# Kernel tuning notes

Measured on AMD Instinct MI355X. Metric: run time of the kernel, lower is better.

The kernel has to match this reference:

```python
import jax, jax.numpy as jnp
import numpy as np

DIM = 384
NH = 12
DH = 32
WH = WW = 7
WS = WH * WW
SCALE = DH ** -0.5


def _relative_position_index(wh, ww):
    # replicates double_step_seq + flip + flatten from the torch module
    seq1 = np.arange(wh) * (2 * ww - 1)
    seq2 = np.arange(ww)
    coords = (seq1[:, None] + seq2[None, :]).reshape(1, -1)  # (1, ws)
    idx = coords + coords.T                                   # (ws, ws)
    idx = idx[:, ::-1]                                        # flip along dim 1
    return jnp.asarray(idx.reshape(-1), dtype=jnp.int32)      # (ws*ws,)

REL_IDX = _relative_position_index(WH, WW)


def setup_inputs() -> dict:
    key = jax.random.key(0)
    k1, k2, k3, k4, k5, k6 = jax.random.split(key, 6)
    x = jax.random.normal(k1, (2048, WS, DIM), dtype=jnp.float32)
    # 0 / -inf style shifted-window mask (use -1e9 for numerical safety)
    u = jax.random.uniform(k2, (64, WS, WS))
    mask = jnp.where(u < 0.1, -1e9, 0.0).astype(jnp.float32)
    inner = NH * DH
    w_qkv = jax.random.normal(k3, (DIM, 3 * inner), dtype=jnp.float32) * 0.02
    bias_table = jax.random.normal(k4, ((2 * WH - 1) * (2 * WW - 1), NH), dtype=jnp.float32) * 0.02
    w_out = jax.random.normal(k5, (inner, DIM), dtype=jnp.float32) * 0.02
    b_out = jax.random.normal(k6, (DIM,), dtype=jnp.float32) * 0.02
    return {"x": x, "mask": mask, "w_qkv": w_qkv, "bias_table": bias_table,
            "w_out": w_out, "b_out": b_out}


def reference(x, mask, w_qkv, bias_table, w_out, b_out):
    b, n, _ = x.shape
    qkv = x @ w_qkv                                  # (b, n, 3*nh*dh)
    q, k, v = jnp.split(qkv, 3, axis=-1)
    def to_heads(t):
        return t.reshape(b, n, NH, DH).transpose(0, 2, 1, 3)  # (b, nh, n, dh)
    q, k, v = to_heads(q) * SCALE, to_heads(k), to_heads(v)
    sim = jnp.einsum('bhid,bhjd->bhij', q, k)        # (b, nh, n, n)
    rel_bias = bias_table[REL_IDX].reshape(WS, WS, NH).transpose(2, 0, 1)  # (nh, n, n)
    sim = sim + rel_bias[None]
    nw = mask.shape[0]
    sim = sim.reshape(b // nw, nw, NH, n, n) + mask[None, :, None]
    sim = sim.reshape(b, NH, n, n)
    attn = jax.nn.softmax(sim, axis=-1)
    out = jnp.einsum('bhij,bhjd->bhid', attn, v)     # (b, nh, n, dh)
    out = out.transpose(0, 2, 1, 3).reshape(b, n, NH * DH)
    return out @ w_out + b_out
```

## Files before the change

kernel.cpp:

```cpp
#include <hip/hip_runtime.h>
#include <hip/hip_bf16.h>
#include <cstdint>
#include <cstddef>

typedef __bf16 bf16_t;
typedef __bf16 bf16x8 __attribute__((ext_vector_type(8)));
typedef __bf16 bf16x4v __attribute__((ext_vector_type(4)));
typedef float f32x4 __attribute__((ext_vector_type(4)));

#define SCALE_Q 0.17677669529663687f


__global__ void conv_x_kernel(const float* __restrict__ x, bf16_t* __restrict__ xb, int n4) {
  int i = blockIdx.x * blockDim.x + threadIdx.x;
  int stride = gridDim.x * blockDim.x;
  const float4* xv = (const float4*)x;
  for (; i < n4; i += stride) {
    float4 v = xv[i];
    bf16x4v o;
    o[0] = (bf16_t)v.x; o[1] = (bf16_t)v.y; o[2] = (bf16_t)v.z; o[3] = (bf16_t)v.w;
    *(bf16x4v*)(xb + (size_t)i * 4) = o;
  }
}

__global__ void conv_small_kernel(const float* __restrict__ w_qkv, const float* __restrict__ w_out,
                                  const float* __restrict__ bias_table, const float* __restrict__ mask,
                                  bf16_t* __restrict__ wqkvt, bf16_t* __restrict__ woutt,
                                  float* __restrict__ rbm) {
  const int N1 = 1152 * 384;
  const int N2 = 384 * 384;
  const int N3 = 64 * 12 * 2401;
  int i = blockIdx.x * blockDim.x + threadIdx.x;
  int stride = gridDim.x * blockDim.x;
  for (; i < N1 + N2 + N3; i += stride) {
    if (i < N1) {
      int n = i / 384, k = i - n * 384;
      wqkvt[i] = (bf16_t)w_qkv[k * 1152 + n];
    } else if (i < N1 + N2) {
      int j = i - N1;
      int n = j / 384, k = j - n * 384;
      woutt[j] = (bf16_t)w_out[k * 384 + n];
    } else {
      int j = i - (N1 + N2);
      int w = j / 28812; int rem = j - w * 28812;
      int h = rem / 2401; int ij = rem - h * 2401;
      int ii = ij / 49; int jj = ij - ii * 49;
      int ci = (ii / 7) * 13 + (ii % 7);
      int j48 = 48 - jj;
      int cj = (j48 / 7) * 13 + (j48 % 7);
      rbm[j] = bias_table[(ci + cj) * 12 + h] + mask[w * 2401 + ij];
    }
  }
}


__global__ __launch_bounds__(256) void gemm_qkv_kernel(const bf16_t* __restrict__ A,
                                                       const bf16_t* __restrict__ Bt,
                                                       bf16_t* __restrict__ Q, bf16_t* __restrict__ K,
                                                       bf16_t* __restrict__ V) {
  __shared__ bf16_t As[128 * 32];
  __shared__ bf16_t Bs[128 * 32];
  int bm = blockIdx.x, bn = blockIdx.y;
  int t = threadIdx.x;
  int lane = t & 63, w = t >> 6, wr = w >> 1, wc = w & 1;
  int m0 = bm * 128, n0 = bn * 128;

  int abase[2], bbase[2];
#pragma unroll
  for (int q = 0; q < 2; ++q) {
    int idx8 = q * 256 + t;
    int r = idx8 >> 2, ko = (idx8 & 3) << 3;
    abase[q] = (m0 + r) * 384 + ko;
    bbase[q] = (n0 + r) * 384 + ko;
  }

  f32x4 acc[4][4] = {};
  int lr = lane & 15, lg = lane >> 4;
  for (int kt = 0; kt < 12; ++kt) {
    int k0 = kt * 32;
#pragma unroll
    for (int q = 0; q < 2; ++q) {
      int idx8 = q * 256 + t;
      *(uint4*)(&As[idx8 * 8]) = *(const uint4*)(&A[abase[q] + k0]);
      *(uint4*)(&Bs[idx8 * 8]) = *(const uint4*)(&Bt[bbase[q] + k0]);
    }
    __syncthreads();
    bf16x8 af[4], bfv[4];
#pragma unroll
    for (int mi = 0; mi < 4; ++mi) af[mi] = *(const bf16x8*)(&As[(wr * 64 + mi * 16 + lr) * 32 + lg * 8]);
#pragma unroll
    for (int ni = 0; ni < 4; ++ni) bfv[ni] = *(const bf16x8*)(&Bs[(wc * 64 + ni * 16 + lr) * 32 + lg * 8]);
#pragma unroll
    for (int mi = 0; mi < 4; ++mi)
#pragma unroll
      for (int ni = 0; ni < 4; ++ni)
        acc[mi][ni] = __builtin_amdgcn_mfma_f32_16x16x32_bf16(af[mi], bfv[ni], acc[mi][ni], 0, 0, 0);
    __syncthreads();
  }

#pragma unroll
  for (int mi = 0; mi < 4; ++mi)
#pragma unroll
    for (int ni = 0; ni < 4; ++ni) {
      int c = n0 + wc * 64 + ni * 16 + lr;
      int part = c / 384;
      int cc = c - part * 384;
      int h = cc >> 5, d = cc & 31;
      bf16_t* dst = (part == 0) ? Q : ((part == 1) ? K : V);
      float sc = (part == 0) ? SCALE_Q : 1.0f;
#pragma unroll
      for (int rg = 0; rg < 4; ++rg) {
        int m = m0 + wr * 64 + mi * 16 + lg * 4 + rg;
        int b = m / 49; int n = m - b * 49;
        dst[((size_t)(b * 12 + h) * 49 + n) * 32 + d] = (bf16_t)(acc[mi][ni][rg] * sc);
      }
    }
}


__global__ __launch_bounds__(64) void attn_kernel(bf16_t* Qio, const bf16_t* __restrict__ Kb,
                                                  const bf16_t* __restrict__ Vb,
                                                  const float* __restrict__ rbm) {
  __shared__ float tbl[49 * 49];
  __shared__ bf16_t Pl[64 * 72];
  __shared__ bf16_t Vt[32 * 72];
  int bh = blockIdx.x;
  int b = bh / 12, h = bh - b * 12;
  int w = b & 63;
  int t = threadIdx.x;
  int lr = t & 15, lg = t >> 4;

  const float* tsrc = rbm + (size_t)(w * 12 + h) * 2401;
  for (int i = t; i < 2401; i += 64) tbl[i] = tsrc[i];
  for (int i = t; i < 32 * 72; i += 64) Vt[i] = (bf16_t)0.0f;
  __syncthreads();

  const bf16_t* vb = Vb + (size_t)bh * 1568;
  for (int ch = t; ch < 196; ch += 64) {
    int row = ch >> 2; int d8 = (ch & 3) << 3;
    bf16x8 vv = *(const bf16x8*)(&vb[row * 32 + d8]);
#pragma unroll
    for (int j = 0; j < 8; ++j) Vt[(d8 + j) * 72 + row] = vv[j];
  }

  const bf16_t* qb = Qio + (size_t)bh * 1568;
  const bf16_t* kb = Kb + (size_t)bh * 1568;
  bf16x8 aq[4], ak[4];
#pragma unroll
  for (int ti = 0; ti < 4; ++ti) { int r = ti * 16 + lr; if (r > 48) r = 48; aq[ti] = *(const bf16x8*)(&qb[r * 32 + lg * 8]); }
#pragma unroll
  for (int tj = 0; tj < 4; ++tj) { int r = tj * 16 + lr; if (r > 48) r = 48; ak[tj] = *(const bf16x8*)(&kb[r * 32 + lg * 8]); }

  f32x4 s[4][4];
#pragma unroll
  for (int ti = 0; ti < 4; ++ti)
#pragma unroll
    for (int tj = 0; tj < 4; ++tj) {
      f32x4 z = {};
      s[ti][tj] = __builtin_amdgcn_mfma_f32_16x16x32_bf16(aq[ti], ak[tj], z, 0, 0, 0);
    }

#pragma unroll
  for (int ti = 0; ti < 4; ++ti)
#pragma unroll
    for (int tj = 0; tj < 4; ++tj)
#pragma unroll
      for (int rg = 0; rg < 4; ++rg) {
        int i = ti * 16 + lg * 4 + rg;
        int j = tj * 16 + lr;
        int ic = i < 49 ? i : 48;
        float add = (j < 49) ? tbl[ic * 49 + j] : -1e30f;
        s[ti][tj][rg] += add;
      }

  float rs[4][4];
#pragma unroll
  for (int ti = 0; ti < 4; ++ti)
#pragma unroll
    for (int rg = 0; rg < 4; ++rg) {
      float mx = fmaxf(fmaxf(s[ti][0][rg], s[ti][1][rg]), fmaxf(s[ti][2][rg], s[ti][3][rg]));
#pragma unroll
      for (int off = 1; off < 16; off <<= 1) mx = fmaxf(mx, __shfl_xor(mx, off));
      float sm = 0.f;
#pragma unroll
      for (int tj = 0; tj < 4; ++tj) {
        float p = __expf(s[ti][tj][rg] - mx);
        s[ti][tj][rg] = p;
        sm += p;
      }
#pragma unroll
      for (int off = 1; off < 16; off <<= 1) sm += __shfl_xor(sm, off);
      rs[ti][rg] = 1.0f / sm;
    }

#pragma unroll
  for (int ti = 0; ti < 4; ++ti)
#pragma unroll
    for (int tj = 0; tj < 4; ++tj)
#pragma unroll
      for (int rg = 0; rg < 4; ++rg) {
        int row = ti * 16 + lg * 4 + rg, col = tj * 16 + lr;
        Pl[row * 72 + col] = (bf16_t)s[ti][tj][rg];
      }
  __syncthreads();

  f32x4 o[4][2] = {};
#pragma unroll
  for (int ks = 0; ks < 2; ++ks) {
    bf16x8 bv[2];
#pragma unroll
    for (int tn = 0; tn < 2; ++tn) bv[tn] = *(const bf16x8*)(&Vt[(tn * 16 + lr) * 72 + ks * 32 + lg * 8]);
#pragma unroll
    for (int ti = 0; ti < 4; ++ti) {
      bf16x8 ap = *(const bf16x8*)(&Pl[(ti * 16 + lr) * 72 + ks * 32 + lg * 8]);
#pragma unroll
      for (int tn = 0; tn < 2; ++tn)
        o[ti][tn] = __builtin_amdgcn_mfma_f32_16x16x32_bf16(ap, bv[tn], o[ti][tn], 0, 0, 0);
    }
  }

  bf16_t* ob = Qio + (size_t)bh * 1568;
#pragma unroll
  for (int ti = 0; ti < 4; ++ti)
#pragma unroll
    for (int tn = 0; tn < 2; ++tn)
#pragma unroll
      for (int rg = 0; rg < 4; ++rg) {
        int row = ti * 16 + lg * 4 + rg;
        if (row < 49) {
          int d = tn * 16 + lr;
          ob[row * 32 + d] = (bf16_t)(o[ti][tn][rg] * rs[ti][rg]);
        }
      }
}


__global__ __launch_bounds__(256) void gemm_out_kernel(const bf16_t* __restrict__ O,
                                                       const bf16_t* __restrict__ Bt,
                                                       const float* __restrict__ bias,
                                                       float* __restrict__ C) {
  __shared__ bf16_t As[128 * 32];
  __shared__ bf16_t Bs[128 * 32];
  int bm = blockIdx.x, bn = blockIdx.y;
  int t = threadIdx.x;
  int lane = t & 63, w = t >> 6, wr = w >> 1, wc = w & 1;
  int m0 = bm * 128, n0 = bn * 128;

  int abase[2], bbase[2];
#pragma unroll
  for (int q = 0; q < 2; ++q) {
    int idx8 = q * 256 + t;
    int r = idx8 >> 2, ko = (idx8 & 3) << 3;
    int m = m0 + r;
    int b = m / 49, n = m - b * 49;
    abase[q] = b * 18816 + n * 32 + ko;
    bbase[q] = (n0 + r) * 384 + ko;
  }

  f32x4 acc[4][4] = {};
  int lr = lane & 15, lg = lane >> 4;
  for (int kt = 0; kt < 12; ++kt) {
#pragma unroll
    for (int q = 0; q < 2; ++q) {
      int idx8 = q * 256 + t;
      *(uint4*)(&As[idx8 * 8]) = *(const uint4*)(&O[abase[q] + kt * 1568]);
      *(uint4*)(&Bs[idx8 * 8]) = *(const uint4*)(&Bt[bbase[q] + kt * 32]);
    }
    __syncthreads();
    bf16x8 af[4], bfv[4];
#pragma unroll
    for (int mi = 0; mi < 4; ++mi) af[mi] = *(const bf16x8*)(&As[(wr * 64 + mi * 16 + lr) * 32 + lg * 8]);
#pragma unroll
    for (int ni = 0; ni < 4; ++ni) bfv[ni] = *(const bf16x8*)(&Bs[(wc * 64 + ni * 16 + lr) * 32 + lg * 8]);
#pragma unroll
    for (int mi = 0; mi < 4; ++mi)
#pragma unroll
      for (int ni = 0; ni < 4; ++ni)
        acc[mi][ni] = __builtin_amdgcn_mfma_f32_16x16x32_bf16(af[mi], bfv[ni], acc[mi][ni], 0, 0, 0);
    __syncthreads();
  }

#pragma unroll
  for (int mi = 0; mi < 4; ++mi)
#pragma unroll
    for (int ni = 0; ni < 4; ++ni) {
      int c = n0 + wc * 64 + ni * 16 + lr;
      float bo = bias[c];
#pragma unroll
      for (int rg = 0; rg < 4; ++rg) {
        int m = m0 + wr * 64 + mi * 16 + lg * 4 + rg;
        C[(size_t)m * 384 + c] = acc[mi][ni][rg] + bo;
      }
    }
}


extern "C" void kernel_launch(void* const* d_in, const int* in_sizes, int n_in,
                              void* d_out, int out_size, void* d_ws, size_t ws_size,
                              hipStream_t stream) {
  const float* x          = (const float*)d_in[0];
  const float* mask       = (const float*)d_in[1];
  const float* w_qkv      = (const float*)d_in[2];
  const float* bias_table = (const float*)d_in[3];
  const float* w_out      = (const float*)d_in[4];
  const float* b_out      = (const float*)d_in[5];
  float* out = (float*)d_out;

  const size_t XE = 38535168ULL;
  char* ws = (char*)d_ws;
  size_t off = 0;
  auto alloc = [&](size_t bytes) { void* p = ws + off; off += (bytes + 255) & ~(size_t)255; return p; };
  bf16_t* xb    = (bf16_t*)alloc(XE * 2);
  bf16_t* wqkvt = (bf16_t*)alloc(442368ULL * 2);
  bf16_t* woutt = (bf16_t*)alloc(147456ULL * 2);
  float*  rbm   = (float*) alloc(1843968ULL * 4);
  bf16_t* Qb    = (bf16_t*)alloc(XE * 2);
  bf16_t* Kb    = (bf16_t*)alloc(XE * 2);
  bf16_t* Vb    = (bf16_t*)alloc(XE * 2);
  if (off > ws_size) return;

  conv_x_kernel<<<2048, 256, 0, stream>>>(x, xb, (int)(XE / 4));
  conv_small_kernel<<<1188, 256, 0, stream>>>(w_qkv, w_out, bias_table, mask, wqkvt, woutt, rbm);
  gemm_qkv_kernel<<<dim3(784, 9), 256, 0, stream>>>(xb, wqkvt, Qb, Kb, Vb);
  attn_kernel<<<24576, 64, 0, stream>>>(Qb, Kb, Vb, rbm);
  gemm_out_kernel<<<dim3(784, 3), 256, 0, stream>>>(Qb, woutt, b_out, out);
}
```

Baseline: 704.7 us.

## Use direct global-to-LDS loads, swizzle block order, and persist attention per window-head

Both GEMM kernels now stage tiles with global_load_lds instead of register round-trips, and remap a flattened 1D block id in an XCD-aware order for better L2 locality. The attention kernel becomes persistent per (window, head): each 128-thread block loads the bias+mask table once and two waves each loop over 16 batches, instead of reloading the 2401-entry table for every (batch, head). In exchange there are fewer blocks (768), so less parallelism to hide latency, plus a per-wave LDS dependency that relies on an explicit waitcnt rather than a barrier.

```diff
diff --git a/kernel.cpp b/kernel.cpp
--- a/kernel.cpp
+++ b/kernel.cpp
@@ -9,6 +9,12 @@
 typedef float f32x4 __attribute__((ext_vector_type(4)));
 
 #define SCALE_Q 0.17677669529663687f
+
+typedef const __attribute__((address_space(1))) unsigned int* gas1;
+typedef __attribute__((address_space(3))) unsigned int* las3;
+__device__ __forceinline__ void gload16(const bf16_t* g, bf16_t* l) {
+  __builtin_amdgcn_global_load_lds((gas1)(const void*)g, (las3)(void*)l, 16, 0, 0);
+}
 
 
 __global__ void conv_x_kernel(const float* __restrict__ x, bf16_t* __restrict__ xb, int n4) {
@@ -58,9 +64,11 @@
                                                        const bf16_t* __restrict__ Bt,
                                                        bf16_t* __restrict__ Q, bf16_t* __restrict__ K,
                                                        bf16_t* __restrict__ V) {
-  __shared__ bf16_t As[128 * 32];
-  __shared__ bf16_t Bs[128 * 32];
-  int bm = blockIdx.x, bn = blockIdx.y;
+  __shared__ __align__(16) bf16_t As[128 * 32];
+  __shared__ __align__(16) bf16_t Bs[128 * 32];
+  int bid = blockIdx.x;
+  int nb = (bid & 7) * 882 + (bid >> 3);
+  int bm = nb / 9, bn = nb - bm * 9;
   int t = threadIdx.x;
   int lane = t & 63, w = t >> 6, wr = w >> 1, wc = w & 1;
   int m0 = bm * 128, n0 = bn * 128;
@@ -78,12 +86,10 @@
   int lr = lane & 15, lg = lane >> 4;
   for (int kt = 0; kt < 12; ++kt) {
     int k0 = kt * 32;
-#pragma unroll
-    for (int q = 0; q < 2; ++q) {
-      int idx8 = q * 256 + t;
-      *(uint4*)(&As[idx8 * 8]) = *(const uint4*)(&A[abase[q] + k0]);
-      *(uint4*)(&Bs[idx8 * 8]) = *(const uint4*)(&Bt[bbase[q] + k0]);
-    }
+    gload16(&A[abase[0] + k0], &As[t * 8]);
+    gload16(&A[abase[1] + k0], &As[(256 + t) * 8]);
+    gload16(&Bt[bbase[0] + k0], &Bs[t * 8]);
+    gload16(&Bt[bbase[1] + k0], &Bs[(256 + t) * 8]);
     __syncthreads();
     bf16x8 af[4], bfv[4];
 #pragma unroll
@@ -118,120 +124,132 @@
 }
 
 
-__global__ __launch_bounds__(64) void attn_kernel(bf16_t* Qio, const bf16_t* __restrict__ Kb,
-                                                  const bf16_t* __restrict__ Vb,
-                                                  const float* __restrict__ rbm) {
-  __shared__ float tbl[49 * 49];
-  __shared__ bf16_t Pl[64 * 72];
-  __shared__ bf16_t Vt[32 * 72];
-  int bh = blockIdx.x;
-  int b = bh / 12, h = bh - b * 12;
-  int w = b & 63;
+__global__ __launch_bounds__(128) void attn_kernel(bf16_t* Qio, const bf16_t* __restrict__ Kb,
+                                                   const bf16_t* __restrict__ Vb,
+                                                   const float* __restrict__ rbm) {
+  __shared__ float tbl[2401];
+  __shared__ __align__(16) bf16_t Pl[2][64 * 72];
+  __shared__ __align__(16) bf16_t Vt[2][32 * 72];
+  int wh = blockIdx.x;
   int t = threadIdx.x;
-  int lr = t & 15, lg = t >> 4;
-
-  const float* tsrc = rbm + (size_t)(w * 12 + h) * 2401;
-  for (int i = t; i < 2401; i += 64) tbl[i] = tsrc[i];
-  for (int i = t; i < 32 * 72; i += 64) Vt[i] = (bf16_t)0.0f;
+  int wv = t >> 6, lane = t & 63;
+  int lr = lane & 15, lg = lane >> 4;
+  int w = wh / 12, h = wh - w * 12;
+
+  const float* tsrc = rbm + (size_t)wh * 2401;
+  for (int i = t; i < 2401; i += 128) tbl[i] = tsrc[i];
+  bf16_t* pl = Pl[wv];
+  bf16_t* vt = Vt[wv];
+  for (int i = lane; i < 32 * 24; i += 64) {
+    int r = i / 24, c = 48 + (i - (i / 24) * 24);
+    vt[r * 72 + c] = (bf16_t)0.0f;
+  }
   __syncthreads();
 
-  const bf16_t* vb = Vb + (size_t)bh * 1568;
-  for (int ch = t; ch < 196; ch += 64) {
-    int row = ch >> 2; int d8 = (ch & 3) << 3;
-    bf16x8 vv = *(const bf16x8*)(&vb[row * 32 + d8]);
-#pragma unroll
-    for (int j = 0; j < 8; ++j) Vt[(d8 + j) * 72 + row] = vv[j];
-  }
-
-  const bf16_t* qb = Qio + (size_t)bh * 1568;
-  const bf16_t* kb = Kb + (size_t)bh * 1568;
-  bf16x8 aq[4], ak[4];
-#pragma unroll
-  for (int ti = 0; ti < 4; ++ti) { int r = ti * 16 + lr; if (r > 48) r = 48; aq[ti] = *(const bf16x8*)(&qb[r * 32 + lg * 8]); }
-#pragma unroll
-  for (int tj = 0; tj < 4; ++tj) { int r = tj * 16 + lr; if (r > 48) r = 48; ak[tj] = *(const bf16x8*)(&kb[r * 32 + lg * 8]); }
-
-  f32x4 s[4][4];
-#pragma unroll
-  for (int ti = 0; ti < 4; ++ti)
-#pragma unroll
-    for (int tj = 0; tj < 4; ++tj) {
-      f32x4 z = {};
-      s[ti][tj] = __builtin_amdgcn_mfma_f32_16x16x32_bf16(aq[ti], ak[tj], z, 0, 0, 0);
-    }
-
-#pragma unroll
-  for (int ti = 0; ti < 4; ++ti)
-#pragma unroll
-    for (int tj = 0; tj < 4; ++tj)
+  for (int it = 0; it < 16; ++it) {
+    int b = w + 64 * (wv * 16 + it);
+    size_t bh = (size_t)b * 12 + h;
+    const bf16_t* qb = Qio + bh * 1568;
+    const bf16_t* kb = Kb + bh * 1568;
+    const bf16_t* vb = Vb + bh * 1568;
+
+    for (int ch = lane; ch < 196; ch += 64) {
+      int row = ch >> 2; int d8 = (ch & 3) << 3;
+      bf16x8 vv = *(const bf16x8*)(&vb[row * 32 + d8]);
+#pragma unroll
+      for (int j = 0; j < 8; ++j) vt[(d8 + j) * 72 + row] = vv[j];
+    }
+
+    bf16x8 aq[4], ak[4];
+#pragma unroll
+    for (int ti = 0; ti < 4; ++ti) {
+      int r = ti * 16 + lr; if (r > 48) r = 48;
+      aq[ti] = *(const bf16x8*)(&qb[r * 32 + lg * 8]);
+      ak[ti] = *(const bf16x8*)(&kb[r * 32 + lg * 8]);
+    }
+
+    f32x4 s[4][4];
+#pragma unroll
+    for (int ti = 0; ti < 4; ++ti)
+#pragma unroll
+      for (int tj = 0; tj < 4; ++tj) {
+        f32x4 z = {};
+        s[ti][tj] = __builtin_amdgcn_mfma_f32_16x16x32_bf16(aq[ti], ak[tj], z, 0, 0, 0);
+      }
+
+#pragma unroll
+    for (int ti = 0; ti < 4; ++ti)
+#pragma unroll
+      for (int tj = 0; tj < 4; ++tj)
+#pragma unroll
+        for (int rg = 0; rg < 4; ++rg) {
+          int i = ti * 16 + lg * 4 + rg;
+          int j = tj * 16 + lr;
+          int ic = i < 49 ? i : 48;
+          float add = (j < 49) ? tbl[ic * 49 + j] : -1e30f;
+          s[ti][tj][rg] += add;
+        }
+
+    float rs[4][4];
+#pragma unroll
+    for (int ti = 0; ti < 4; ++ti)
 #pragma unroll
       for (int rg = 0; rg < 4; ++rg) {
-        int i = ti * 16 + lg * 4 + rg;
-        int j = tj * 16 + lr;
-        int ic = i < 49 ? i : 48;
-        float add = (j < 49) ? tbl[ic * 49 + j] : -1e30f;
-        s[ti][tj][rg] += add;
-      }
-
-  float rs[4][4];
-#pragma unroll
-  for (int ti = 0; ti < 4; ++ti)
-#pragma unroll
-    for (int rg = 0; rg < 4; ++rg) {
-      float mx = fmaxf(fmaxf(s[ti][0][rg], s[ti][1][rg]), fmaxf(s[ti][2][rg], s[ti][3][rg]));
-#pragma unroll
-      for (int off = 1; off < 16; off <<= 1) mx = fmaxf(mx, __shfl_xor(mx, off));
-      float sm = 0.f;
-#pragma unroll
-      for (int tj = 0; tj < 4; ++tj) {
-        float p = __expf(s[ti][tj][rg] - mx);
-        s[ti][tj][rg] = p;
-        sm += p;
-      }
-#pragma unroll
-      for (int off = 1; off < 16; off <<= 1) sm += __shfl_xor(sm, off);
-      rs[ti][rg] = 1.0f / sm;
-    }
-
-#pragma unroll
-  for (int ti = 0; ti < 4; ++ti)
-#pragma unroll
-    for (int tj = 0; tj < 4; ++tj)
-#pragma unroll
-      for (int rg = 0; rg < 4; ++rg) {
-        int row = ti * 16 + lg * 4 + rg, col = tj * 16 + lr;
-        Pl[row * 72 + col] = (bf16_t)s[ti][tj][rg];
-      }
-  __syncthreads();
-
-  f32x4 o[4][2] = {};
-#pragma unroll
-  for (int ks = 0; ks < 2; ++ks) {
-    bf16x8 bv[2];
-#pragma unroll
-    for (int tn = 0; tn < 2; ++tn) bv[tn] = *(const bf16x8*)(&Vt[(tn * 16 + lr) * 72 + ks * 32 + lg * 8]);
-#pragma unroll
-    for (int ti = 0; ti < 4; ++ti) {
-      bf16x8 ap = *(const bf16x8*)(&Pl[(ti * 16 + lr) * 72 + ks * 32 + lg * 8]);
+        float mx = fmaxf(fmaxf(s[ti][0][rg], s[ti][1][rg]), fmaxf(s[ti][2][rg], s[ti][3][rg]));
+#pragma unroll
+        for (int off = 1; off < 16; off <<= 1) mx = fmaxf(mx, __shfl_xor(mx, off));
+        float sm = 0.f;
+#pragma unroll
+        for (int tj = 0; tj < 4; ++tj) {
+          float p = __expf(s[ti][tj][rg] - mx);
+          s[ti][tj][rg] = p;
+          sm += p;
+        }
+#pragma unroll
+        for (int off = 1; off < 16; off <<= 1) sm += __shfl_xor(sm, off);
+        rs[ti][rg] = 1.0f / sm;
+      }
+
+#pragma unroll
+    for (int ti = 0; ti < 4; ++ti)
+#pragma unroll
+      for (int tj = 0; tj < 4; ++tj)
+#pragma unroll
+        for (int rg = 0; rg < 4; ++rg) {
+          int row = ti * 16 + lg * 4 + rg, col = tj * 16 + lr;
+          pl[row * 72 + col] = (bf16_t)s[ti][tj][rg];
+        }
+    asm volatile("s_waitcnt lgkmcnt(0)" ::: "memory");
+
+    f32x4 o[4][2] = {};
+#pragma unroll
+    for (int ks = 0; ks < 2; ++ks) {
+      bf16x8 bv[2];
+#pragma unroll
+      for (int tn = 0; tn < 2; ++tn) bv[tn] = *(const bf16x8*)(&vt[(tn * 16 + lr) * 72 + ks * 32 + lg * 8]);
+#pragma unroll
+      for (int ti = 0; ti < 4; ++ti) {
+        bf16x8 ap = *(const bf16x8*)(&pl[(ti * 16 + lr) * 72 + ks * 32 + lg * 8]);
+#pragma unroll
+        for (int tn = 0; tn < 2; ++tn)
+          o[ti][tn] = __builtin_amdgcn_mfma_f32_16x16x32_bf16(ap, bv[tn], o[ti][tn], 0, 0, 0);
+      }
+    }
+
+    bf16_t* ob = Qio + bh * 1568;
+#pragma unroll
+    for (int ti = 0; ti < 4; ++ti)
 #pragma unroll
       for (int tn = 0; tn < 2; ++tn)
-        o[ti][tn] = __builtin_amdgcn_mfma_f32_16x16x32_bf16(ap, bv[tn], o[ti][tn], 0, 0, 0);
-    }
-  }
-
-  bf16_t* ob = Qio + (size_t)bh * 1568;
-#pragma unroll
-  for (int ti = 0; ti < 4; ++ti)
-#pragma unroll
-    for (int tn = 0; tn < 2; ++tn)
-#pragma unroll
-      for (int rg = 0; rg < 4; ++rg) {
-        int row = ti * 16 + lg * 4 + rg;
-        if (row < 49) {
-          int d = tn * 16 + lr;
-          ob[row * 32 + d] = (bf16_t)(o[ti][tn][rg] * rs[ti][rg]);
+#pragma unroll
+        for (int rg = 0; rg < 4; ++rg) {
+          int row = ti * 16 + lg * 4 + rg;
+          if (row < 49) {
+            int d = tn * 16 + lr;
+            ob[row * 32 + d] = (bf16_t)(o[ti][tn][rg] * rs[ti][rg]);
+          }
         }
-      }
+  }
 }
 
 
@@ -239,9 +257,11 @@
                                                        const bf16_t* __restrict__ Bt,
                                                        const float* __restrict__ bias,
                                                        float* __restrict__ C) {
-  __shared__ bf16_t As[128 * 32];
-  __shared__ bf16_t Bs[128 * 32];
-  int bm = blockIdx.x, bn = blockIdx.y;
+  __shared__ __align__(16) bf16_t As[128 * 32];
+  __shared__ __align__(16) bf16_t Bs[128 * 32];
+  int bid = blockIdx.x;
+  int nb = (bid & 7) * 294 + (bid >> 3);
+  int bm = nb / 3, bn = nb - bm * 3;
   int t = threadIdx.x;
   int lane = t & 63, w = t >> 6, wr = w >> 1, wc = w & 1;
   int m0 = bm * 128, n0 = bn * 128;
@@ -260,12 +280,10 @@
   f32x4 acc[4][4] = {};
   int lr = lane & 15, lg = lane >> 4;
   for (int kt = 0; kt < 12; ++kt) {
-#pragma unroll
-    for (int q = 0; q < 2; ++q) {
-      int idx8 = q * 256 + t;
-      *(uint4*)(&As[idx8 * 8]) = *(const uint4*)(&O[abase[q] + kt * 1568]);
-      *(uint4*)(&Bs[idx8 * 8]) = *(const uint4*)(&Bt[bbase[q] + kt * 32]);
-    }
+    gload16(&O[abase[0] + kt * 1568], &As[t * 8]);
+    gload16(&O[abase[1] + kt * 1568], &As[(256 + t) * 8]);
+    gload16(&Bt[bbase[0] + kt * 32], &Bs[t * 8]);
+    gload16(&Bt[bbase[1] + kt * 32], &Bs[(256 + t) * 8]);
     __syncthreads();
     bf16x8 af[4], bfv[4];
 #pragma unroll
@@ -321,7 +339,7 @@
 
   conv_x_kernel<<<2048, 256, 0, stream>>>(x, xb, (int)(XE / 4));
   conv_small_kernel<<<1188, 256, 0, stream>>>(w_qkv, w_out, bias_table, mask, wqkvt, woutt, rbm);
-  gemm_qkv_kernel<<<dim3(784, 9), 256, 0, stream>>>(xb, wqkvt, Qb, Kb, Vb);
-  attn_kernel<<<24576, 64, 0, stream>>>(Qb, Kb, Vb, rbm);
-  gemm_out_kernel<<<dim3(784, 3), 256, 0, stream>>>(Qb, woutt, b_out, out);
-}
+  gemm_qkv_kernel<<<7056, 256, 0, stream>>>(xb, wqkvt, Qb, Kb, Vb);
+  attn_kernel<<<768, 128, 0, stream>>>(Qb, Kb, Vb, rbm);
+  gemm_out_kernel<<<2352, 256, 0, stream>>>(Qb, woutt, b_out, out);
+}
```

Measured after the change: 631.3 us. 1.12x faster.
